# Performance work log

Measured on AMD Instinct MI355X. Metric: run time of the kernel, lower is better.

## Reference

```python
import jax, jax.numpy as jnp
import numpy as np

N, L, D_MODEL, NUM_HEADS, MAX_SEQ = 4, 1024, 1024, 16, 2048
DEPTH = D_MODEL // NUM_HEADS


def setup_inputs() -> dict:
    key = jax.random.key(0)
    ks = jax.random.split(key, 12)
    inv = 1.0 / np.sqrt(D_MODEL)
    inp = {
        "q_in": jax.random.normal(ks[0], (N, L, D_MODEL), jnp.float32),
        "k_in": jax.random.normal(ks[1], (N, L, D_MODEL), jnp.float32),
        "v_in": jax.random.normal(ks[2], (N, L, D_MODEL), jnp.float32),
        # causal additive mask: 1.0 where attention is disallowed (j > i)
        "mask": (jnp.triu(jnp.ones((L, L), jnp.float32), k=1))[None, None, :, :],
        "Wq": jax.random.normal(ks[3], (D_MODEL, D_MODEL), jnp.float32) * inv,
        "bq": jnp.zeros((D_MODEL,), jnp.float32),
        "Wk": jax.random.normal(ks[4], (D_MODEL, D_MODEL), jnp.float32) * inv,
        "bk": jnp.zeros((D_MODEL,), jnp.float32),
        "Wv": jax.random.normal(ks[5], (D_MODEL, D_MODEL), jnp.float32) * inv,
        "bv": jnp.zeros((D_MODEL,), jnp.float32),
        "Wo": jax.random.normal(ks[6], (D_MODEL, D_MODEL), jnp.float32) * inv,
        "bo": jnp.zeros((D_MODEL,), jnp.float32),
        "pos_emb": jax.random.normal(ks[7], (MAX_SEQ, DEPTH), jnp.float32) * 0.02,
    }
    return inp


def _rel_bias(q, pos_emb):
    """q: [N,H,L,depth] -> skewed relative-position bias s: [N,H,L,L]."""
    n, h, l, d = q.shape
    e = pos_emb[pos_emb.shape[0] - l:, :]                     # [L, depth]
    qe = jnp.einsum('nhld,md->nhlm', q, e)                    # [N,H,L,L]
    # keep only the last (i+1) entries of row i (upper-left triangle zeroed)
    m = qe.shape[-1]
    keep = (jnp.arange(m)[None, :] >= (m - 1 - jnp.arange(l))[:, None]).astype(qe.dtype)
    qe = qe * keep
    # skew via pad/reshape/slice
    padded = jnp.pad(qe, ((0, 0), (0, 0), (0, 0), (1, 0)))    # [N,H,L,L+1]
    s = padded.reshape(n, h, l + 1, l)[:, :, 1:, :]           # [N,H,L,L]
    return s


def reference(q_in, k_in, v_in, mask, Wq, bq, Wk, bk, Wv, bv, Wo, bo, pos_emb):
    n, l, dm = q_in.shape
    h, d = NUM_HEADS, DEPTH

    def split(x):
        return x.reshape(n, l, h, d).transpose(0, 2, 1, 3)    # [N,H,L,depth]

    q = split(q_in @ Wq + bq)
    k = split(k_in @ Wk + bk)
    v = split(v_in @ Wv + bv)

    s = _rel_bias(q, pos_emb)
    logits = (jnp.einsum('nhld,nhmd->nhlm', q, k) + s) / jnp.sqrt(jnp.float32(d))
    logits = logits + mask * (-1e9)
    attn = jax.nn.softmax(logits, axis=-1)                    # [N,H,L,L]
    out = jnp.einsum('nhlm,nhmd->nhld', attn, v)
    out = out.transpose(0, 2, 1, 3).reshape(n, l, dm)
    return out @ Wo + bo
```

## Files before the change

### kernel.cpp

```cpp
#include <hip/hip_runtime.h>

typedef unsigned short u16t;
typedef unsigned int   u32t;
typedef __bf16 bf16x8 __attribute__((ext_vector_type(8)));
typedef float  f32x4  __attribute__((ext_vector_type(4)));

#define NB     4
#define SEQ    1024
#define DMODEL 1024
#define NHEAD  16
#define DEPTH  64
#define MAXSEQ 2048
#define MTOK   (NB * SEQ)

#define AS1 __attribute__((address_space(1)))
#define AS3 __attribute__((address_space(3)))

__device__ __forceinline__ u16t f2bf(float f) {
  u32t u = __builtin_bit_cast(u32t, f);
  u32t r = (u + 0x7fffu + ((u >> 16) & 1u)) >> 16;
  return (u16t)r;
}
__device__ __forceinline__ float bf2f(u16t h) {
  return __builtin_bit_cast(float, (u32t)h << 16);
}
__device__ __forceinline__ void load_lds16(const void* g, void* l) {
  __builtin_amdgcn_global_load_lds((AS1 u32t*)(g), (AS3 u32t*)(l), 16, 0, 0);
}

__global__ void cvt3_kernel(const float* __restrict__ a, const float* __restrict__ b,
                            const float* __restrict__ c,
                            u16t* __restrict__ oa, u16t* __restrict__ ob,
                            u16t* __restrict__ oc, int n8) {
  int i = blockIdx.x * blockDim.x + threadIdx.x;
  if (i >= n8) return;
  const float* src = (blockIdx.z == 0) ? a : ((blockIdx.z == 1) ? b : c);
  u16t* dst = (blockIdx.z == 0) ? oa : ((blockIdx.z == 1) ? ob : oc);
  const float4* s4 = (const float4*)src;
  float4 x = s4[2 * i], y = s4[2 * i + 1];
  u16t tmp[8] = { f2bf(x.x), f2bf(x.y), f2bf(x.z), f2bf(x.w),
                  f2bf(y.x), f2bf(y.y), f2bf(y.z), f2bf(y.w) };
  ((uint4*)dst)[i] = *(const uint4*)tmp;
}

__global__ void transpose4_kernel(const float* __restrict__ w0, const float* __restrict__ w1,
                                  const float* __restrict__ w2, const float* __restrict__ w3,
                                  u16t* __restrict__ t0, u16t* __restrict__ t1,
                                  u16t* __restrict__ t2, u16t* __restrict__ t3) {
  const int z = blockIdx.z;
  const float* W = (z == 0) ? w0 : ((z == 1) ? w1 : ((z == 2) ? w2 : w3));
  u16t* WT = (z == 0) ? t0 : ((z == 1) ? t1 : ((z == 2) ? t2 : t3));
  __shared__ float tile[32][33];
  const int tx = threadIdx.x & 31, ty = threadIdx.x >> 5;
  const int bx = blockIdx.x * 32, by = blockIdx.y * 32;
#pragma unroll
  for (int r = 0; r < 32; r += 8)
    tile[ty + r][tx] = W[(size_t)(by + ty + r) * DMODEL + bx + tx];
  __syncthreads();
#pragma unroll
  for (int r = 0; r < 32; r += 8)
    WT[(size_t)(bx + ty + r) * DMODEL + by + tx] = f2bf(tile[tx][ty + r]);
}

__global__ void erel_kernel(const float* __restrict__ pe, u16t* __restrict__ Er) {
  int idx = blockIdx.x * blockDim.x + threadIdx.x;
  int r = idx >> 6, d = idx & 63;
  Er[idx] = f2bf(pe[(size_t)(MAXSEQ - 1 - r) * DEPTH + d]);
}

template <typename OutT>
__device__ __forceinline__ void gemm_bt_body(
    const u16t* __restrict__ A, const u16t* __restrict__ BT,
    const float* __restrict__ bias, OutT* __restrict__ C,
    int M, int Nc, int K, int bx, int by, float scale) {
  __shared__ __align__(16) u16t As[128 * 32];
  __shared__ __align__(16) u16t Bs[128 * 32];
  const int tid = threadIdx.x;
  const int wave = tid >> 6;
  const int lane = tid & 63;
  const int q = lane >> 4, t = lane & 15;
  const int lrow = lane >> 2, lch = lane & 3;
  const int bm = by * 128, bn = bx * 128;
  const int wi = (wave >> 1) * 64, wj = (wave & 1) * 64;

  f32x4 acc[4][4];
#pragma unroll
  for (int i = 0; i < 4; ++i)
#pragma unroll
    for (int j = 0; j < 4; ++j) acc[i][j] = f32x4{0.f, 0.f, 0.f, 0.f};

  for (int kt = 0; kt < K; kt += 32) {
    __syncthreads();
#pragma unroll
    for (int it = 0; it < 2; ++it) {
      const int rb = it * 64 + wave * 16;
      const u16t* ga = A + (size_t)(bm + rb + lrow) * K + kt + lch * 8;
      const u16t* gb = BT + (size_t)(bn + rb + lrow) * K + kt + lch * 8;
      load_lds16(ga, As + rb * 32);
      load_lds16(gb, Bs + rb * 32);
    }
    __syncthreads();
    bf16x8 af[4], bfr[4];
#pragma unroll
    for (int i = 0; i < 4; ++i) {
      af[i]  = *(const bf16x8*)(As + (wi + i * 16 + t) * 32 + q * 8);
      bfr[i] = *(const bf16x8*)(Bs + (wj + i * 16 + t) * 32 + q * 8);
    }
#pragma unroll
    for (int i = 0; i < 4; ++i)
#pragma unroll
      for (int j = 0; j < 4; ++j)
        acc[i][j] = __builtin_amdgcn_mfma_f32_16x16x32_bf16(af[i], bfr[j], acc[i][j], 0, 0, 0);
  }
#pragma unroll
  for (int j = 0; j < 4; ++j) {
    const int col = bn + wj + j * 16 + t;
    const float bv = bias[col];
#pragma unroll
    for (int i = 0; i < 4; ++i) {
#pragma unroll
      for (int r = 0; r < 4; ++r) {
        const int row = bm + wi + i * 16 + q * 4 + r;
        float v = (acc[i][j][r] + bv) * scale;
        if constexpr (sizeof(OutT) == 2) {
          C[(size_t)row * Nc + col] = f2bf(v);
        } else {
          C[(size_t)row * Nc + col] = v;
        }
      }
    }
  }
}

__global__ __launch_bounds__(256) void gemm_qkv_kernel(
    const u16t* qa, const u16t* ka, const u16t* va,
    const u16t* wq, const u16t* wk, const u16t* wv,
    const float* bq, const float* bk, const float* bv,
    u16t* qo, u16t* ko, u16t* vo) {
  const int z = blockIdx.z;
  const u16t* A = (z == 0) ? qa : ((z == 1) ? ka : va);
  const u16t* B = (z == 0) ? wq : ((z == 1) ? wk : wv);
  const float* bb = (z == 0) ? bq : ((z == 1) ? bk : bv);
  u16t* C = (z == 0) ? qo : ((z == 1) ? ko : vo);
  const float scale = (z == 0) ? 0.125f : 1.0f;
  gemm_bt_body<u16t>(A, B, bb, C, MTOK, DMODEL, DMODEL, blockIdx.x, blockIdx.y, scale);
}

__global__ __launch_bounds__(256) void gemm_out_kernel(
    const u16t* __restrict__ A, const u16t* __restrict__ W,
    const float* __restrict__ bias, float* __restrict__ C) {
  gemm_bt_body<float>(A, W, bias, C, MTOK, DMODEL, DMODEL, blockIdx.x, blockIdx.y, 1.0f);
}

__global__ __launch_bounds__(256) void attn_kernel(
    const u16t* __restrict__ Qp, const u16t* __restrict__ Kp, const u16t* __restrict__ Vp,
    const u16t* __restrict__ Er, u16t* __restrict__ AO) {
  const int p = blockIdx.x;
  const int h = blockIdx.y;
  const int n = blockIdx.z;
  const int tid = threadIdx.x;
  const int wave = tid >> 6, lane = tid & 63;
  const int q = lane >> 4, t = lane & 15;

  __shared__ __align__(16) u16t Ks[64 * 64];
  __shared__ __align__(16) u16t Es[128 * 64];
  __shared__ __align__(16) u16t Vt[64 * 64];
  __shared__ __align__(16) u16t TP[4 * 2112];

  const int rr = tid >> 3;
  const int c0 = (tid & 7) * 8;
  u16t* TPw = TP + wave * 2112;

#pragma unroll
  for (int ph = 0; ph < 2; ++ph) {
    const int bx = ph ? p : (15 - p);
    const int I0 = bx * 64;
    const int iw = I0 + wave * 16;
    const size_t qoff = ((size_t)(n * SEQ + iw + t)) * DMODEL + h * DEPTH;
    const bf16x8 qf0 = *(const bf16x8*)(Qp + qoff + q * 8);
    const bf16x8 qf1 = *(const bf16x8*)(Qp + qoff + 32 + q * 8);

    f32x4 o[4];
#pragma unroll
    for (int c = 0; c < 4; ++c) o[c] = f32x4{0.f, 0.f, 0.f, 0.f};
    float l_r[4] = {0.f, 0.f, 0.f, 0.f};

    for (int jt = 0; jt <= bx; ++jt) {
      const int J0 = jt * 64;
      const int rbase = I0 - J0 - 63;
      __syncthreads();
#pragma unroll
      for (int it = 0; it < 2; ++it) {
        const int chunk = it * 256 + tid;
        const int j = chunk >> 3, d8 = (chunk & 7) * 8;
        const u16t* g = Kp + ((size_t)(n * SEQ + J0 + j)) * DMODEL + h * DEPTH + d8;
        load_lds16(g, Ks + (it * 256 + wave * 64) * 8);
      }
      const u16t* Eb = Er + (ptrdiff_t)rbase * DEPTH;
#pragma unroll
      for (int it = 0; it < 4; ++it) {
        const int chunk = it * 256 + tid;
        const int rc = chunk >> 3, d8 = (chunk & 7) * 8;
        const u16t* g = Eb + (ptrdiff_t)rc * DEPTH + d8;
        load_lds16(g, Es + (it * 256 + wave * 64) * 8);
      }
#pragma unroll
      for (int rep = 0; rep < 2; ++rep) {
        const int j = rr + rep * 32;
        const size_t goff = ((size_t)(n * SEQ + J0 + j)) * DMODEL + h * DEPTH + c0;
        uint4 vv = *(const uint4*)(Vp + goff);
        const u16t* pv = (const u16t*)&vv;
#pragma unroll
        for (int u = 0; u < 8; ++u) {
          const int d = c0 + u;
          Vt[d * 64 + (j ^ (((d >> 2) & 7) << 3))] = pv[u];
        }
      }
      __syncthreads();

      f32x4 s[4], tb[8];
#pragma unroll
      for (int c = 0; c < 4; ++c) s[c] = f32x4{0.f, 0.f, 0.f, 0.f};
#pragma unroll
      for (int c = 0; c < 8; ++c) tb[c] = f32x4{0.f, 0.f, 0.f, 0.f};
#pragma unroll
      for (int kk = 0; kk < 2; ++kk) {
        const bf16x8 qf = kk ? qf1 : qf0;
#pragma unroll
        for (int c = 0; c < 4; ++c) {
          bf16x8 kf = *(const bf16x8*)(Ks + (c * 16 + t) * 64 + kk * 32 + q * 8);
          s[c] = __builtin_amdgcn_mfma_f32_16x16x32_bf16(qf, kf, s[c], 0, 0, 0);
        }
#pragma unroll
        for (int c = 0; c < 8; ++c) {
          bf16x8 ef = *(const bf16x8*)(Es + (c * 16 + t) * 64 + kk * 32 + q * 8);
          tb[c] = __builtin_amdgcn_mfma_f32_16x16x32_bf16(qf, ef, tb[c], 0, 0, 0);
        }
      }
#pragma unroll
      for (int c = 0; c < 8; ++c)
#pragma unroll
        for (int r = 0; r < 4; ++r)
          TPw[(q * 4 + r) * 132 + c * 16 + t] = f2bf(tb[c][r]);

      const int mneed = 63 - 64 * (bx - jt);
      const int tbase = wave * 16 + q * 4 + 63 - t;
#pragma unroll
      for (int c = 0; c < 4; ++c) {
#pragma unroll
        for (int r = 0; r < 4; ++r) {
          const int idx = tbase + r - c * 16;
          float lg = s[c][r] + bf2f(TPw[(q * 4 + r) * 132 + idx]);
          lg = (idx >= mneed) ? lg : -1e30f;
          const float pr = __expf(lg);
          s[c][r] = pr;
          l_r[r] += pr;
        }
      }
#pragma unroll
      for (int c = 0; c < 4; ++c)
#pragma unroll
        for (int r = 0; r < 4; ++r)
          TPw[(q * 4 + r) * 72 + c * 16 + t] = f2bf(s[c][r]);

      const bf16x8 pf0 = *(const bf16x8*)(TPw + t * 72 + q * 8);
      const bf16x8 pf1 = *(const bf16x8*)(TPw + t * 72 + 32 + q * 8);
#pragma unroll
      for (int c2 = 0; c2 < 4; ++c2) {
        const int dd = c2 * 16 + t;
        const int sw = (dd >> 2) & 7;
        const bf16x8 v0 = *(const bf16x8*)(Vt + dd * 64 + ((0 + q) ^ sw) * 8);
        const bf16x8 v1 = *(const bf16x8*)(Vt + dd * 64 + ((4 + q) ^ sw) * 8);
        o[c2] = __builtin_amdgcn_mfma_f32_16x16x32_bf16(pf0, v0, o[c2], 0, 0, 0);
        o[c2] = __builtin_amdgcn_mfma_f32_16x16x32_bf16(pf1, v1, o[c2], 0, 0, 0);
      }
    }

#pragma unroll
    for (int r = 0; r < 4; ++r) {
      float lsum = l_r[r];
      lsum += __shfl_xor(lsum, 1, 64);
      lsum += __shfl_xor(lsum, 2, 64);
      lsum += __shfl_xor(lsum, 4, 64);
      lsum += __shfl_xor(lsum, 8, 64);
      const float inv = 1.f / lsum;
      const size_t obase = ((size_t)(n * SEQ + iw + q * 4 + r)) * DMODEL + h * DEPTH;
#pragma unroll
      for (int c2 = 0; c2 < 4; ++c2)
        AO[obase + c2 * 16 + t] = f2bf(o[c2][r] * inv);
    }
  }
}

extern "C" void kernel_launch(void* const* d_in, const int* in_sizes, int n_in,
                              void* d_out, int out_size, void* d_ws, size_t ws_size,
                              hipStream_t stream) {
  const float* q_in = (const float*)d_in[0];
  const float* k_in = (const float*)d_in[1];
  const float* v_in = (const float*)d_in[2];
  const float* Wq = (const float*)d_in[4];
  const float* bq = (const float*)d_in[5];
  const float* Wk = (const float*)d_in[6];
  const float* bk = (const float*)d_in[7];
  const float* Wv = (const float*)d_in[8];
  const float* bv = (const float*)d_in[9];
  const float* Wo = (const float*)d_in[10];
  const float* bo = (const float*)d_in[11];
  const float* pe = (const float*)d_in[12];
  float* out = (float*)d_out;

  char* ws = (char*)d_ws;
  constexpr size_t MB = 1ull << 20;
  u16t* qb  = (u16t*)(ws);
  u16t* kb  = (u16t*)(ws + 8 * MB);
  u16t* vb  = (u16t*)(ws + 16 * MB);
  u16t* Erl = (u16t*)(ws + 24 * MB);
  u16t* Qp  = (u16t*)(ws + 26 * MB);
  u16t* Kp  = (u16t*)(ws + 34 * MB);
  u16t* Vp  = (u16t*)(ws + 42 * MB);
  u16t* AOb = (u16t*)(ws + 50 * MB);
  u16t* WqT = (u16t*)(ws + 58 * MB);
  u16t* WkT = (u16t*)(ws + 60 * MB);
  u16t* WvT = (u16t*)(ws + 62 * MB);
  u16t* WoT = (u16t*)(ws + 64 * MB);

  const size_t SZA = (size_t)MTOK * DMODEL;
  const int n8 = (int)(SZA / 8);
  cvt3_kernel<<<dim3(n8 / 256, 1, 3), 256, 0, stream>>>(q_in, k_in, v_in, qb, kb, vb, n8);
  transpose4_kernel<<<dim3(32, 32, 4), 256, 0, stream>>>(Wq, Wk, Wv, Wo, WqT, WkT, WvT, WoT);
  erel_kernel<<<(SEQ * DEPTH) / 256, 256, 0, stream>>>(pe, Erl);

  gemm_qkv_kernel<<<dim3(DMODEL / 128, MTOK / 128, 3), 256, 0, stream>>>(
      qb, kb, vb, WqT, WkT, WvT, bq, bk, bv, Qp, Kp, Vp);

  attn_kernel<<<dim3(8, NHEAD, NB), 256, 0, stream>>>(Qp, Kp, Vp, Erl, AOb);

  gemm_out_kernel<<<dim3(DMODEL / 128, MTOK / 128, 1), 256, 0, stream>>>(AOb, WoT, bo, out);
}
```

Measured before the change: 259.4 us.

## Reschedule attention grid per XCD, reuse relative-position rows, fold erel into transpose

The attention kernel drops the paired-row-block scheme (two query tiles per block) and launches 1024 single-tile blocks. The flat index is remapped so that heads sharing an XCD land together, with the longest tiles scheduled first. The Er relative-position tile becomes a 128-row ring buffer: after the first tile only 64 new rows are loaded per step, halving those loads. V global loads are issued before the barrier so their latency overlaps the sync, and the erel conversion is merged into the transpose launch to save one kernel launch. This trades the balanced per-block work of the paired scheme for more blocks and relies on the hardware scheduler to balance the longest-first ordering.

```diff
diff --git a/kernel.cpp b/kernel.cpp
--- a/kernel.cpp
+++ b/kernel.cpp
@@ -46,8 +46,18 @@
 __global__ void transpose4_kernel(const float* __restrict__ w0, const float* __restrict__ w1,
                                   const float* __restrict__ w2, const float* __restrict__ w3,
                                   u16t* __restrict__ t0, u16t* __restrict__ t1,
-                                  u16t* __restrict__ t2, u16t* __restrict__ t3) {
+                                  u16t* __restrict__ t2, u16t* __restrict__ t3,
+                                  const float* __restrict__ pe, u16t* __restrict__ Er) {
   const int z = blockIdx.z;
+  if (z == 4) {
+    const int flat = blockIdx.y * 32 + blockIdx.x;
+    if (flat < 256) {
+      const int idx = flat * 256 + threadIdx.x;
+      const int r = idx >> 6, d = idx & 63;
+      Er[idx] = f2bf(pe[(size_t)(MAXSEQ - 1 - r) * DEPTH + d]);
+    }
+    return;
+  }
   const float* W = (z == 0) ? w0 : ((z == 1) ? w1 : ((z == 2) ? w2 : w3));
   u16t* WT = (z == 0) ? t0 : ((z == 1) ? t1 : ((z == 2) ? t2 : t3));
   __shared__ float tile[32][33];
@@ -60,12 +70,6 @@
 #pragma unroll
   for (int r = 0; r < 32; r += 8)
     WT[(size_t)(bx + ty + r) * DMODEL + by + tx] = f2bf(tile[tx][ty + r]);
-}
-
-__global__ void erel_kernel(const float* __restrict__ pe, u16t* __restrict__ Er) {
-  int idx = blockIdx.x * blockDim.x + threadIdx.x;
-  int r = idx >> 6, d = idx & 63;
-  Er[idx] = f2bf(pe[(size_t)(MAXSEQ - 1 - r) * DEPTH + d]);
 }
 
 template <typename OutT>
@@ -155,9 +159,12 @@
 __global__ __launch_bounds__(256) void attn_kernel(
     const u16t* __restrict__ Qp, const u16t* __restrict__ Kp, const u16t* __restrict__ Vp,
     const u16t* __restrict__ Er, u16t* __restrict__ AO) {
-  const int p = blockIdx.x;
-  const int h = blockIdx.y;
-  const int n = blockIdx.z;
+  const int gx = blockIdx.x;
+  const int slot = gx >> 3, xcd = gx & 7;
+  const int g = ((slot >> 4) << 3) | xcd;
+  const int bx = 15 - (slot & 15);
+  const int n = g >> 4, h = g & 15;
+
   const int tid = threadIdx.x;
   const int wave = tid >> 6, lane = tid & 63;
   const int q = lane >> 4, t = lane & 15;
@@ -171,124 +178,137 @@
   const int c0 = (tid & 7) * 8;
   u16t* TPw = TP + wave * 2112;
 
-#pragma unroll
-  for (int ph = 0; ph < 2; ++ph) {
-    const int bx = ph ? p : (15 - p);
-    const int I0 = bx * 64;
-    const int iw = I0 + wave * 16;
-    const size_t qoff = ((size_t)(n * SEQ + iw + t)) * DMODEL + h * DEPTH;
-    const bf16x8 qf0 = *(const bf16x8*)(Qp + qoff + q * 8);
-    const bf16x8 qf1 = *(const bf16x8*)(Qp + qoff + 32 + q * 8);
-
-    f32x4 o[4];
-#pragma unroll
-    for (int c = 0; c < 4; ++c) o[c] = f32x4{0.f, 0.f, 0.f, 0.f};
-    float l_r[4] = {0.f, 0.f, 0.f, 0.f};
-
-    for (int jt = 0; jt <= bx; ++jt) {
-      const int J0 = jt * 64;
-      const int rbase = I0 - J0 - 63;
-      __syncthreads();
+  const int I0 = bx * 64;
+  const int iw = I0 + wave * 16;
+  const size_t qoff = ((size_t)(n * SEQ + iw + t)) * DMODEL + h * DEPTH;
+  const bf16x8 qf0 = *(const bf16x8*)(Qp + qoff + q * 8);
+  const bf16x8 qf1 = *(const bf16x8*)(Qp + qoff + 32 + q * 8);
+
+  f32x4 o[4];
+#pragma unroll
+  for (int c = 0; c < 4; ++c) o[c] = f32x4{0.f, 0.f, 0.f, 0.f};
+  float l_r[4] = {0.f, 0.f, 0.f, 0.f};
+
+  for (int jt = 0; jt <= bx; ++jt) {
+    const int J0 = jt * 64;
+    const int rbase = I0 - J0 - 63;
+    const int s0 = ((bx - jt) & 1) << 6;
+
+    const size_t vgo = ((size_t)(n * SEQ + J0 + rr)) * DMODEL + h * DEPTH + c0;
+    const uint4 vv0 = *(const uint4*)(Vp + vgo);
+    const uint4 vv1 = *(const uint4*)(Vp + vgo + 32 * DMODEL);
+
+    __syncthreads();
+
+#pragma unroll
+    for (int it = 0; it < 2; ++it) {
+      const int chunk = it * 256 + tid;
+      const int j = chunk >> 3, d8 = (chunk & 7) * 8;
+      const u16t* gk = Kp + ((size_t)(n * SEQ + J0 + j)) * DMODEL + h * DEPTH + d8;
+      load_lds16(gk, Ks + (it * 256 + wave * 64) * 8);
+    }
+    const u16t* Eb = Er + (ptrdiff_t)rbase * DEPTH;
+    if (jt == 0) {
+#pragma unroll
+      for (int it = 0; it < 4; ++it) {
+        const int rc = it * 32 + (tid >> 3);
+        const int dst = ((s0 + it * 32) & 127) * 64;
+        load_lds16(Eb + (ptrdiff_t)rc * DEPTH + c0,
+                   Es + dst + wave * 64 * 8);
+      }
+    } else {
 #pragma unroll
       for (int it = 0; it < 2; ++it) {
-        const int chunk = it * 256 + tid;
-        const int j = chunk >> 3, d8 = (chunk & 7) * 8;
-        const u16t* g = Kp + ((size_t)(n * SEQ + J0 + j)) * DMODEL + h * DEPTH + d8;
-        load_lds16(g, Ks + (it * 256 + wave * 64) * 8);
-      }
-      const u16t* Eb = Er + (ptrdiff_t)rbase * DEPTH;
-#pragma unroll
-      for (int it = 0; it < 4; ++it) {
-        const int chunk = it * 256 + tid;
-        const int rc = chunk >> 3, d8 = (chunk & 7) * 8;
-        const u16t* g = Eb + (ptrdiff_t)rc * DEPTH + d8;
-        load_lds16(g, Es + (it * 256 + wave * 64) * 8);
-      }
-#pragma unroll
-      for (int rep = 0; rep < 2; ++rep) {
-        const int j = rr + rep * 32;
-        const size_t goff = ((size_t)(n * SEQ + J0 + j)) * DMODEL + h * DEPTH + c0;
-        uint4 vv = *(const uint4*)(Vp + goff);
-        const u16t* pv = (const u16t*)&vv;
-#pragma unroll
-        for (int u = 0; u < 8; ++u) {
-          const int d = c0 + u;
-          Vt[d * 64 + (j ^ (((d >> 2) & 7) << 3))] = pv[u];
-        }
-      }
-      __syncthreads();
-
-      f32x4 s[4], tb[8];
-#pragma unroll
-      for (int c = 0; c < 4; ++c) s[c] = f32x4{0.f, 0.f, 0.f, 0.f};
-#pragma unroll
-      for (int c = 0; c < 8; ++c) tb[c] = f32x4{0.f, 0.f, 0.f, 0.f};
-#pragma unroll
-      for (int kk = 0; kk < 2; ++kk) {
-        const bf16x8 qf = kk ? qf1 : qf0;
-#pragma unroll
-        for (int c = 0; c < 4; ++c) {
-          bf16x8 kf = *(const bf16x8*)(Ks + (c * 16 + t) * 64 + kk * 32 + q * 8);
-          s[c] = __builtin_amdgcn_mfma_f32_16x16x32_bf16(qf, kf, s[c], 0, 0, 0);
-        }
-#pragma unroll
-        for (int c = 0; c < 8; ++c) {
-          bf16x8 ef = *(const bf16x8*)(Es + (c * 16 + t) * 64 + kk * 32 + q * 8);
-          tb[c] = __builtin_amdgcn_mfma_f32_16x16x32_bf16(qf, ef, tb[c], 0, 0, 0);
-        }
-      }
-#pragma unroll
-      for (int c = 0; c < 8; ++c)
-#pragma unroll
-        for (int r = 0; r < 4; ++r)
-          TPw[(q * 4 + r) * 132 + c * 16 + t] = f2bf(tb[c][r]);
-
-      const int mneed = 63 - 64 * (bx - jt);
-      const int tbase = wave * 16 + q * 4 + 63 - t;
+        const int rc = it * 32 + (tid >> 3);
+        const int dst = (s0 + it * 32) * 64;
+        load_lds16(Eb + (ptrdiff_t)rc * DEPTH + c0,
+                   Es + dst + wave * 64 * 8);
+      }
+    }
+    {
+      const u16t* pv0 = (const u16t*)&vv0;
+      const u16t* pv1 = (const u16t*)&vv1;
+#pragma unroll
+      for (int u = 0; u < 8; ++u) {
+        const int d = c0 + u;
+        const int sh = ((d >> 2) & 7) << 3;
+        Vt[d * 64 + (rr ^ sh)] = pv0[u];
+        Vt[d * 64 + ((rr + 32) ^ sh)] = pv1[u];
+      }
+    }
+    __syncthreads();
+
+    f32x4 s[4], tb[8];
+#pragma unroll
+    for (int c = 0; c < 4; ++c) s[c] = f32x4{0.f, 0.f, 0.f, 0.f};
+#pragma unroll
+    for (int c = 0; c < 8; ++c) tb[c] = f32x4{0.f, 0.f, 0.f, 0.f};
+#pragma unroll
+    for (int kk = 0; kk < 2; ++kk) {
+      const bf16x8 qf = kk ? qf1 : qf0;
 #pragma unroll
       for (int c = 0; c < 4; ++c) {
-#pragma unroll
-        for (int r = 0; r < 4; ++r) {
-          const int idx = tbase + r - c * 16;
-          float lg = s[c][r] + bf2f(TPw[(q * 4 + r) * 132 + idx]);
-          lg = (idx >= mneed) ? lg : -1e30f;
-          const float pr = __expf(lg);
-          s[c][r] = pr;
-          l_r[r] += pr;
-        }
-      }
-#pragma unroll
-      for (int c = 0; c < 4; ++c)
-#pragma unroll
-        for (int r = 0; r < 4; ++r)
-          TPw[(q * 4 + r) * 72 + c * 16 + t] = f2bf(s[c][r]);
-
-      const bf16x8 pf0 = *(const bf16x8*)(TPw + t * 72 + q * 8);
-      const bf16x8 pf1 = *(const bf16x8*)(TPw + t * 72 + 32 + q * 8);
-#pragma unroll
-      for (int c2 = 0; c2 < 4; ++c2) {
-        const int dd = c2 * 16 + t;
-        const int sw = (dd >> 2) & 7;
-        const bf16x8 v0 = *(const bf16x8*)(Vt + dd * 64 + ((0 + q) ^ sw) * 8);
-        const bf16x8 v1 = *(const bf16x8*)(Vt + dd * 64 + ((4 + q) ^ sw) * 8);
-        o[c2] = __builtin_amdgcn_mfma_f32_16x16x32_bf16(pf0, v0, o[c2], 0, 0, 0);
-        o[c2] = __builtin_amdgcn_mfma_f32_16x16x32_bf16(pf1, v1, o[c2], 0, 0, 0);
-      }
-    }
-
-#pragma unroll
-    for (int r = 0; r < 4; ++r) {
-      float lsum = l_r[r];
-      lsum += __shfl_xor(lsum, 1, 64);
-      lsum += __shfl_xor(lsum, 2, 64);
-      lsum += __shfl_xor(lsum, 4, 64);
-      lsum += __shfl_xor(lsum, 8, 64);
-      const float inv = 1.f / lsum;
-      const size_t obase = ((size_t)(n * SEQ + iw + q * 4 + r)) * DMODEL + h * DEPTH;
-#pragma unroll
-      for (int c2 = 0; c2 < 4; ++c2)
-        AO[obase + c2 * 16 + t] = f2bf(o[c2][r] * inv);
-    }
+        bf16x8 kf = *(const bf16x8*)(Ks + (c * 16 + t) * 64 + kk * 32 + q * 8);
+        s[c] = __builtin_amdgcn_mfma_f32_16x16x32_bf16(qf, kf, s[c], 0, 0, 0);
+      }
+#pragma unroll
+      for (int c = 0; c < 8; ++c) {
+        const int er = (s0 + c * 16 + t) & 127;
+        bf16x8 ef = *(const bf16x8*)(Es + er * 64 + kk * 32 + q * 8);
+        tb[c] = __builtin_amdgcn_mfma_f32_16x16x32_bf16(qf, ef, tb[c], 0, 0, 0);
+      }
+    }
+#pragma unroll
+    for (int c = 0; c < 8; ++c)
+#pragma unroll
+      for (int r = 0; r < 4; ++r)
+        TPw[(q * 4 + r) * 132 + c * 16 + t] = f2bf(tb[c][r]);
+
+    const int mneed = 63 - 64 * (bx - jt);
+    const int tbase = wave * 16 + q * 4 + 63 - t;
+#pragma unroll
+    for (int c = 0; c < 4; ++c) {
+#pragma unroll
+      for (int r = 0; r < 4; ++r) {
+        const int idx = tbase + r - c * 16;
+        float lg = s[c][r] + bf2f(TPw[(q * 4 + r) * 132 + idx]);
+        lg = (idx >= mneed) ? lg : -1e30f;
+        const float pr = __expf(lg);
+        s[c][r] = pr;
+        l_r[r] += pr;
+      }
+    }
+#pragma unroll
+    for (int c = 0; c < 4; ++c)
+#pragma unroll
+      for (int r = 0; r < 4; ++r)
+        TPw[(q * 4 + r) * 72 + c * 16 + t] = f2bf(s[c][r]);
+
+    const bf16x8 pf0 = *(const bf16x8*)(TPw + t * 72 + q * 8);
+    const bf16x8 pf1 = *(const bf16x8*)(TPw + t * 72 + 32 + q * 8);
+#pragma unroll
+    for (int c2 = 0; c2 < 4; ++c2) {
+      const int dd = c2 * 16 + t;
+      const int sw = (dd >> 2) & 7;
+      const bf16x8 v0 = *(const bf16x8*)(Vt + dd * 64 + ((0 + q) ^ sw) * 8);
+      const bf16x8 v1 = *(const bf16x8*)(Vt + dd * 64 + ((4 + q) ^ sw) * 8);
+      o[c2] = __builtin_amdgcn_mfma_f32_16x16x32_bf16(pf0, v0, o[c2], 0, 0, 0);
+      o[c2] = __builtin_amdgcn_mfma_f32_16x16x32_bf16(pf1, v1, o[c2], 0, 0, 0);
+    }
+  }
+
+#pragma unroll
+  for (int r = 0; r < 4; ++r) {
+    float lsum = l_r[r];
+    lsum += __shfl_xor(lsum, 1, 64);
+    lsum += __shfl_xor(lsum, 2, 64);
+    lsum += __shfl_xor(lsum, 4, 64);
+    lsum += __shfl_xor(lsum, 8, 64);
+    const float inv = 1.f / lsum;
+    const size_t obase = ((size_t)(n * SEQ + iw + q * 4 + r)) * DMODEL + h * DEPTH;
+#pragma unroll
+    for (int c2 = 0; c2 < 4; ++c2)
+      AO[obase + c2 * 16 + t] = f2bf(o[c2][r] * inv);
   }
 }
 
@@ -327,13 +347,13 @@
   const size_t SZA = (size_t)MTOK * DMODEL;
   const int n8 = (int)(SZA / 8);
   cvt3_kernel<<<dim3(n8 / 256, 1, 3), 256, 0, stream>>>(q_in, k_in, v_in, qb, kb, vb, n8);
-  transpose4_kernel<<<dim3(32, 32, 4), 256, 0, stream>>>(Wq, Wk, Wv, Wo, WqT, WkT, WvT, WoT);
-  erel_kernel<<<(SEQ * DEPTH) / 256, 256, 0, stream>>>(pe, Erl);
+  transpose4_kernel<<<dim3(32, 32, 5), 256, 0, stream>>>(Wq, Wk, Wv, Wo, WqT, WkT, WvT, WoT,
+                                                         pe, Erl);
 
   gemm_qkv_kernel<<<dim3(DMODEL / 128, MTOK / 128, 3), 256, 0, stream>>>(
       qb, kb, vb, WqT, WkT, WvT, bq, bk, bv, Qp, Kp, Vp);
 
-  attn_kernel<<<dim3(8, NHEAD, NB), 256, 0, stream>>>(Qp, Kp, Vp, Erl, AOb);
+  attn_kernel<<<dim3(1024, 1, 1), 256, 0, stream>>>(Qp, Kp, Vp, Erl, AOb);
 
   gemm_out_kernel<<<dim3(DMODEL / 128, MTOK / 128, 1), 256, 0, stream>>>(AOb, WoT, bo, out);
 }
```

Measured after the change: 279.6 us. 1.08x slower.
